# Kernel tuning notes

Hardware: AMD Instinct MI355X
Metric: run time of the kernel (lower is better)

Reference implementation:

```python
import jax, jax.numpy as jnp
import numpy as np

ALPHA = 1.0
EPS = 1e-6


def setup_inputs() -> dict:
    key = jax.random.key(0)
    ks = jax.random.split(key, 6)
    B, d_lat, hidden, n_genes = 256, 32, 512, 4000
    z = jax.random.normal(ks[0], (B, d_lat), dtype=jnp.float32)
    W1 = jax.random.normal(ks[1], (d_lat, hidden), dtype=jnp.float32) / np.sqrt(d_lat)
    b1 = jnp.zeros((hidden,), dtype=jnp.float32)
    W2 = jax.random.normal(ks[2], (hidden, n_genes), dtype=jnp.float32) / np.sqrt(hidden)
    b2 = jnp.zeros((n_genes,), dtype=jnp.float32)
    log_theta = 0.5 * jax.random.normal(ks[3], (n_genes,), dtype=jnp.float32)
    return {"z": z, "W1": W1, "b1": b1, "W2": W2, "b2": b2, "log_theta": log_theta}


def _decode_mu(z_vec, W1, b1, W2, b2):
    # NB decoder mean for a single latent vector; lib_dummy == 1 so no scaling.
    h = jax.nn.relu(z_vec @ W1 + b1)            # [hidden]
    return jax.nn.softplus(h @ W2 + b2)          # [n_genes]


def reference(z, W1, b1, W2, b2, log_theta):
    d_lat = z.shape[1]
    theta = jnp.exp(log_theta)                   # [G], per-gene dispersion

    f = lambda zv: _decode_mu(zv, W1, b1, W2, b2)

    mu = jax.vmap(f)(z)                          # [B, G]
    J = jax.vmap(jax.jacfwd(f))(z)               # [B, G, d_lat]

    # weights computed under no_grad in the original
    mu_ng = jax.lax.stop_gradient(mu)
    weights = theta / (mu_ng * (mu_ng + theta) + EPS)   # [B, G]

    # Gram[b, i, j] = sum_g J[b,g,i] * w[b,g] * J[b,g,j]  (== U @ U.T with U = sqrt(w)*J^T)
    Gram = jnp.einsum('bgi,bg,bgj->bij', J, weights, J)  # [B, d_lat, d_lat]

    eye = jnp.eye(d_lat, dtype=z.dtype)
    losses = jnp.sum((Gram - ALPHA * eye) ** 2, axis=(1, 2))  # [B]
    return jnp.mean(losses)
```

## Files before the change

### kernel.cpp

```cpp
#include <hip/hip_runtime.h>

typedef __bf16 bf16x8 __attribute__((ext_vector_type(8)));
typedef float f32x4 __attribute__((ext_vector_type(4)));
typedef unsigned short u16x8 __attribute__((ext_vector_type(8)));

typedef const void __attribute__((address_space(1)))* gas_ptr;
typedef void __attribute__((address_space(3)))* las_ptr;

#define GLOAD16(gp, lp) __builtin_amdgcn_global_load_lds((gas_ptr)(gp), (las_ptr)(lp), 16, 0, 0)

__device__ __forceinline__ unsigned short f2bf(float f) {
  unsigned int u = __float_as_uint(f);
  u += 0x7FFF + ((u >> 16) & 1);
  return (unsigned short)(u >> 16);
}
__device__ __forceinline__ float bf2f(unsigned short u) {
  return __uint_as_float(((unsigned int)u) << 16);
}

__global__ __launch_bounds__(256) void k_w2t(const float* __restrict__ W2,
                                             unsigned short* __restrict__ W2T) {
  __shared__ float tile[64][65];
  const int gt = blockIdx.x;
  const int jt = blockIdx.y;
  const int t = threadIdx.x;
  const int c = t & 63, r4 = t >> 6;
#pragma unroll
  for (int r = 0; r < 16; ++r) {
    int jj = r * 4 + r4;
    int g = gt * 64 + c;
    tile[jj][c] = (g < 4000) ? W2[(size_t)(jt * 64 + jj) * 4000 + g] : 0.f;
  }
  __syncthreads();
#pragma unroll
  for (int r = 0; r < 16; ++r) {
    int gg = r * 4 + r4;
    W2T[(size_t)(gt * 64 + gg) * 512 + jt * 64 + c] = f2bf(tile[c][gg]);
  }
}

__global__ __launch_bounds__(256) void k_mask(const float* __restrict__ z,
                                              const float* __restrict__ W1,
                                              const float* __restrict__ b1,
                                              unsigned char* __restrict__ maskb,
                                              unsigned short* __restrict__ Hb) {
  __shared__ float zs[32];
  const int b = blockIdx.x, t = threadIdx.x;
  if (t < 32) zs[t] = z[b * 32 + t];
  __syncthreads();
#pragma unroll
  for (int jj = 0; jj < 2; ++jj) {
    int j = t + jj * 256;
    float a = b1[j];
#pragma unroll
    for (int i = 0; i < 32; ++i) a = fmaf(zs[i], W1[i * 512 + j], a);
    bool m = a > 0.f;
    maskb[b * 512 + j] = m ? 1 : 0;
    Hb[b * 512 + j] = m ? f2bf(a) : (unsigned short)0;
  }
}

__global__ __launch_bounds__(256) void k_abig(const float* __restrict__ W1,
                                              const unsigned char* __restrict__ maskb,
                                              unsigned short* __restrict__ Astack) {
  const int b = blockIdx.x, t = threadIdx.x;
#pragma unroll
  for (int k = 0; k < 8; ++k) {
    int c8 = t + k * 256;
    int row = c8 >> 6;
    int k8 = (c8 & 63) * 8;
    unsigned long long m8 = *(const unsigned long long*)(maskb + b * 512 + k8);
    const float* w = W1 + row * 512 + k8;
    u16x8 out;
#pragma unroll
    for (int e = 0; e < 8; ++e)
      out[e] = ((m8 >> (e * 8)) & 0xffULL) ? f2bf(w[e]) : (unsigned short)0;
    *(u16x8*)(Astack + ((size_t)(b * 32 + row)) * 512 + k8) = out;
  }
}

__global__ __launch_bounds__(256) void k_s(const unsigned short* __restrict__ Hb,
                                           const unsigned short* __restrict__ W2T,
                                           const float* __restrict__ b2,
                                           const float* __restrict__ log_theta,
                                           float* __restrict__ Cw) {
  __shared__ __align__(16) char smem[49152];
  char* Abuf = smem;
  char* Bbuf = smem + 16384;

  const int bm = blockIdx.x;
  const int g0 = blockIdx.y * 128;
  const int t = threadIdx.x;
  const int lane = t & 63;
  const int wave = t >> 6;
  const int l8 = lane >> 3;
  const int kxor = (((lane & 7) ^ l8) << 3);
  const int c16 = lane & 15;
  const int lg = lane >> 4;

  f32x4 acc[4][2];
#pragma unroll
  for (int mt = 0; mt < 4; ++mt)
#pragma unroll
    for (int nt = 0; nt < 2; ++nt) acc[mt][nt] = (f32x4){0.f, 0.f, 0.f, 0.f};

#define STAGE_S(buf, kt)                                                              \
  do {                                                                                \
    _Pragma("unroll") for (int qq = 0; qq < 2; ++qq) {                                \
      int q = wave * 2 + qq;                                                          \
      GLOAD16(Hb + (size_t)(bm * 64 + q * 8 + l8) * 512 + (kt) * 64 + kxor,           \
              Abuf + (buf) * 8192 + q * 1024);                                        \
    }                                                                                 \
    _Pragma("unroll") for (int qq = 0; qq < 4; ++qq) {                                \
      int q = wave * 4 + qq;                                                          \
      GLOAD16(W2T + (size_t)(g0 + q * 8 + l8) * 512 + (kt) * 64 + kxor,               \
              Bbuf + (buf) * 16384 + q * 1024);                                       \
    }                                                                                 \
  } while (0)

  STAGE_S(0, 0);
  __syncthreads();

  for (int kt = 0; kt < 8; ++kt) {
    int cur = kt & 1;
    if (kt < 7) STAGE_S(cur ^ 1, kt + 1);
    const char* Ab = Abuf + cur * 8192;
    const char* Bb = Bbuf + cur * 16384;
#pragma unroll
    for (int ks = 0; ks < 2; ++ks) {
      int kb = ks * 64 + lg * 16;
      bf16x8 av[4], bv[2];
#pragma unroll
      for (int mt = 0; mt < 4; ++mt) {
        int row = mt * 16 + c16;
        av[mt] = *(const bf16x8*)(Ab + (row >> 3) * 1024 + (row & 7) * 128 + (kb ^ ((row & 7) << 4)));
      }
#pragma unroll
      for (int nt = 0; nt < 2; ++nt) {
        int row = wave * 32 + nt * 16 + c16;
        bv[nt] = *(const bf16x8*)(Bb + (row >> 3) * 1024 + (row & 7) * 128 + (kb ^ ((row & 7) << 4)));
      }
#pragma unroll
      for (int mt = 0; mt < 4; ++mt)
#pragma unroll
        for (int nt = 0; nt < 2; ++nt)
          acc[mt][nt] = __builtin_amdgcn_mfma_f32_16x16x32_bf16(av[mt], bv[nt], acc[mt][nt], 0, 0, 0);
    }
    __syncthreads();
  }

#pragma unroll
  for (int nt = 0; nt < 2; ++nt) {
    int g = g0 + wave * 32 + nt * 16 + c16;
    if (g < 4000) {
      float bb = b2[g];
      float theta = expf(log_theta[g]);
#pragma unroll
      for (int mt = 0; mt < 4; ++mt)
#pragma unroll
        for (int r = 0; r < 4; ++r) {
          int sample = bm * 64 + mt * 16 + lg * 4 + r;
          float s = acc[mt][nt][r] + bb;
          float sig = 1.f / (1.f + expf(-s));
          float mu = (s > 20.f) ? s : log1pf(expf(s));
          float w = theta / (mu * (mu + theta) + 1e-6f);
          Cw[(size_t)sample * 4096 + g] = w * sig * sig;
        }
    } else {
#pragma unroll
      for (int mt = 0; mt < 4; ++mt)
#pragma unroll
        for (int r = 0; r < 4; ++r) {
          int sample = bm * 64 + mt * 16 + lg * 4 + r;
          Cw[(size_t)sample * 4096 + g] = 0.f;
        }
    }
  }
}

__global__ __launch_bounds__(256, 2) void k_gemm(const unsigned short* __restrict__ Astack,
                                                 const unsigned short* __restrict__ W2T,
                                                 const float* __restrict__ Cw,
                                                 float* __restrict__ Gram) {
  __shared__ __align__(16) char smem[65536];
  char* AbufB = smem;
  char* BbufB = smem + 32768;

  const int bm = blockIdx.x;
  const int g0 = blockIdx.y * 128;
  const int t = threadIdx.x;
  const int lane = t & 63;
  const int wave = t >> 6;
  const int wr = wave >> 1, wc = wave & 1;
  const int l8 = lane >> 3;
  const int kxor = (((lane & 7) ^ l8) << 3);
  const int c16 = lane & 15;
  const int lg = lane >> 4;

  f32x4 acc[4][4];
#pragma unroll
  for (int mt = 0; mt < 4; ++mt)
#pragma unroll
    for (int nt = 0; nt < 4; ++nt) acc[mt][nt] = (f32x4){0.f, 0.f, 0.f, 0.f};

  const size_t Abase = (size_t)bm * 128 * 512;

#define STAGE_G(buf, kt)                                                              \
  do {                                                                                \
    _Pragma("unroll") for (int qq = 0; qq < 4; ++qq) {                                \
      int q = wave * 4 + qq;                                                          \
      GLOAD16(Astack + Abase + (size_t)(q * 8 + l8) * 512 + (kt) * 64 + kxor,         \
              AbufB + (buf) * 16384 + q * 1024);                                      \
    }                                                                                 \
    _Pragma("unroll") for (int qq = 0; qq < 4; ++qq) {                                \
      int q = wave * 4 + qq;                                                          \
      GLOAD16(W2T + (size_t)(g0 + q * 8 + l8) * 512 + (kt) * 64 + kxor,               \
              BbufB + (buf) * 16384 + q * 1024);                                      \
    }                                                                                 \
  } while (0)

  STAGE_G(0, 0);
  __syncthreads();

  for (int kt = 0; kt < 8; ++kt) {
    int cur = kt & 1;
    if (kt < 7) STAGE_G(cur ^ 1, kt + 1);
    const char* Ab = AbufB + cur * 16384;
    const char* Bb = BbufB + cur * 16384;
#pragma unroll
    for (int ks = 0; ks < 2; ++ks) {
      int kb = ks * 64 + lg * 16;
      bf16x8 av[4], bv[4];
#pragma unroll
      for (int mt = 0; mt < 4; ++mt) {
        int row = wr * 64 + mt * 16 + c16;
        av[mt] = *(const bf16x8*)(Ab + (row >> 3) * 1024 + (row & 7) * 128 + (kb ^ ((row & 7) << 4)));
      }
#pragma unroll
      for (int nt = 0; nt < 4; ++nt) {
        int row = wc * 64 + nt * 16 + c16;
        bv[nt] = *(const bf16x8*)(Bb + (row >> 3) * 1024 + (row & 7) * 128 + (kb ^ ((row & 7) << 4)));
      }
#pragma unroll
      for (int mt = 0; mt < 4; ++mt)
#pragma unroll
        for (int nt = 0; nt < 4; ++nt)
          acc[mt][nt] = __builtin_amdgcn_mfma_f32_16x16x32_bf16(av[mt], bv[nt], acc[mt][nt], 0, 0, 0);
    }
    __syncthreads();
  }

  unsigned short* T = (unsigned short*)smem;
  float* c_lds = (float*)(smem + 34816);

#pragma unroll
  for (int mt = 0; mt < 4; ++mt)
#pragma unroll
    for (int nt = 0; nt < 4; ++nt)
#pragma unroll
      for (int r = 0; r < 4; ++r) {
        int row = wr * 64 + mt * 16 + lg * 4 + r;
        int col = wc * 64 + nt * 16 + c16;
        T[row * 136 + col] = f2bf(acc[mt][nt][r]);
      }
#pragma unroll
  for (int k = 0; k < 2; ++k) {
    int e = t + k * 256;
    c_lds[e] = Cw[(size_t)(bm * 4 + (e >> 7)) * 4096 + g0 + (e & 127)];
  }
  __syncthreads();

  {
    const int s = wave;
    f32x4 gacc[2][2];
#pragma unroll
    for (int m2 = 0; m2 < 2; ++m2)
#pragma unroll
      for (int n2 = 0; n2 < 2; ++n2) gacc[m2][n2] = (f32x4){0.f, 0.f, 0.f, 0.f};

#pragma unroll
    for (int ch = 0; ch < 4; ++ch) {
      u16x8 raw[2];
      bf16x8 ap[2], bp[2];
      f32x4 cv0 = *(const f32x4*)(c_lds + s * 128 + ch * 32 + lg * 8);
      f32x4 cv1 = *(const f32x4*)(c_lds + s * 128 + ch * 32 + lg * 8 + 4);
#pragma unroll
      for (int m2 = 0; m2 < 2; ++m2) {
        int row = s * 32 + m2 * 16 + c16;
        raw[m2] = *(const u16x8*)((const char*)T + row * 272 + ch * 64 + lg * 16);
        u16x8 sc;
#pragma unroll
        for (int e = 0; e < 4; ++e) sc[e] = f2bf(bf2f(raw[m2][e]) * cv0[e]);
#pragma unroll
        for (int e = 0; e < 4; ++e) sc[4 + e] = f2bf(bf2f(raw[m2][4 + e]) * cv1[e]);
        ap[m2] = __builtin_bit_cast(bf16x8, sc);
        bp[m2] = __builtin_bit_cast(bf16x8, raw[m2]);
      }
#pragma unroll
      for (int m2 = 0; m2 < 2; ++m2)
#pragma unroll
        for (int n2 = 0; n2 < 2; ++n2)
          gacc[m2][n2] = __builtin_amdgcn_mfma_f32_16x16x32_bf16(ap[m2], bp[n2], gacc[m2][n2], 0, 0, 0);
    }

#pragma unroll
    for (int m2 = 0; m2 < 2; ++m2)
#pragma unroll
      for (int n2 = 0; n2 < 2; ++n2)
#pragma unroll
        for (int r = 0; r < 4; ++r) {
          int i = m2 * 16 + lg * 4 + r;
          int j = n2 * 16 + c16;
          atomicAdd(Gram + (size_t)(bm * 4 + s) * 1024 + i * 32 + j, gacc[m2][n2][r]);
        }
  }
}

__global__ __launch_bounds__(256) void k_loss(const float* __restrict__ Gram,
                                              float* __restrict__ out) {
  __shared__ float red[4];
  const int b = blockIdx.x, t = threadIdx.x;
  float local = 0.f;
#pragma unroll
  for (int k = 0; k < 4; ++k) {
    int e = t + k * 256;
    float d = Gram[(size_t)b * 1024 + e] - (((e >> 5) == (e & 31)) ? 1.f : 0.f);
    local += d * d;
  }
#pragma unroll
  for (int off = 32; off > 0; off >>= 1) local += __shfl_down(local, off);
  if ((t & 63) == 0) red[t >> 6] = local;
  __syncthreads();
  if (t == 0) {
    float s = red[0] + red[1] + red[2] + red[3];
    atomicAdd(out, s * (1.f / 256.f));
  }
}

extern "C" void kernel_launch(void* const* d_in, const int* in_sizes, int n_in,
                              void* d_out, int out_size, void* d_ws, size_t ws_size,
                              hipStream_t stream) {
  const float* z = (const float*)d_in[0];
  const float* W1 = (const float*)d_in[1];
  const float* b1 = (const float*)d_in[2];
  const float* W2 = (const float*)d_in[3];
  const float* b2 = (const float*)d_in[4];
  const float* lt = (const float*)d_in[5];

  char* ws = (char*)d_ws;
  unsigned short* W2T = (unsigned short*)ws;
  unsigned short* Astack = (unsigned short*)(ws + 4194304);
  unsigned short* Hb = (unsigned short*)(ws + 12582912);
  unsigned char* maskb = (unsigned char*)(ws + 12845056);
  float* Cw = (float*)(ws + 12976128);
  float* Gram = (float*)(ws + 17170432);

  hipMemsetAsync(Gram, 0, 256 * 1024 * 4, stream);
  hipMemsetAsync(d_out, 0, 4, stream);

  k_w2t<<<dim3(64, 8), 256, 0, stream>>>(W2, W2T);
  k_mask<<<256, 256, 0, stream>>>(z, W1, b1, maskb, Hb);
  k_abig<<<256, 256, 0, stream>>>(W1, maskb, Astack);
  k_s<<<dim3(4, 32), 256, 0, stream>>>(Hb, W2T, b2, lt, Cw);
  k_gemm<<<dim3(64, 32), 256, 0, stream>>>(Astack, W2T, Cw, Gram);
  k_loss<<<256, 256, 0, stream>>>(Gram, (float*)d_out);
}
```

Baseline: 166.0 us.

## Rewrite pre-activation GEMM as per-wave register tiles without LDS staging

Replaces the LDS-staged, double-buffered 64x128 block GEMM in the weight-computation kernel with a per-wave 16x32 tile. Each wave keeps its full K slice of A in registers and streams B directly from global memory. The grid grows from 128 blocks to 512 blocks, so more CUs have work and the LDS and barrier overhead goes away. The cost is less data reuse across waves, more global and L2 traffic for W2T, and higher register pressure from holding 16 A vectors.

Result: faster. 159.9 us (-3.7%).

```diff
diff --git a/kernel.cpp b/kernel.cpp
--- a/kernel.cpp
+++ b/kernel.cpp
@@ -79,101 +79,62 @@
   }
 }
 
-__global__ __launch_bounds__(256) void k_s(const unsigned short* __restrict__ Hb,
-                                           const unsigned short* __restrict__ W2T,
-                                           const float* __restrict__ b2,
-                                           const float* __restrict__ log_theta,
-                                           float* __restrict__ Cw) {
-  __shared__ __align__(16) char smem[49152];
-  char* Abuf = smem;
-  char* Bbuf = smem + 16384;
-
-  const int bm = blockIdx.x;
-  const int g0 = blockIdx.y * 128;
+__global__ __launch_bounds__(256) void k_s2(const unsigned short* __restrict__ Hb,
+                                            const unsigned short* __restrict__ W2T,
+                                            const float* __restrict__ b2,
+                                            const float* __restrict__ log_theta,
+                                            float* __restrict__ Cw) {
   const int t = threadIdx.x;
   const int lane = t & 63;
   const int wave = t >> 6;
-  const int l8 = lane >> 3;
-  const int kxor = (((lane & 7) ^ l8) << 3);
-  const int c16 = lane & 15;
-  const int lg = lane >> 4;
-
-  f32x4 acc[4][2];
-#pragma unroll
-  for (int mt = 0; mt < 4; ++mt)
-#pragma unroll
-    for (int nt = 0; nt < 2; ++nt) acc[mt][nt] = (f32x4){0.f, 0.f, 0.f, 0.f};
-
-#define STAGE_S(buf, kt)                                                              \
-  do {                                                                                \
-    _Pragma("unroll") for (int qq = 0; qq < 2; ++qq) {                                \
-      int q = wave * 2 + qq;                                                          \
-      GLOAD16(Hb + (size_t)(bm * 64 + q * 8 + l8) * 512 + (kt) * 64 + kxor,           \
-              Abuf + (buf) * 8192 + q * 1024);                                        \
-    }                                                                                 \
-    _Pragma("unroll") for (int qq = 0; qq < 4; ++qq) {                                \
-      int q = wave * 4 + qq;                                                          \
-      GLOAD16(W2T + (size_t)(g0 + q * 8 + l8) * 512 + (kt) * 64 + kxor,               \
-              Bbuf + (buf) * 16384 + q * 1024);                                       \
-    }                                                                                 \
-  } while (0)
-
-  STAGE_S(0, 0);
-  __syncthreads();
-
-  for (int kt = 0; kt < 8; ++kt) {
-    int cur = kt & 1;
-    if (kt < 7) STAGE_S(cur ^ 1, kt + 1);
-    const char* Ab = Abuf + cur * 8192;
-    const char* Bb = Bbuf + cur * 16384;
-#pragma unroll
-    for (int ks = 0; ks < 2; ++ks) {
-      int kb = ks * 64 + lg * 16;
-      bf16x8 av[4], bv[2];
-#pragma unroll
-      for (int mt = 0; mt < 4; ++mt) {
-        int row = mt * 16 + c16;
-        av[mt] = *(const bf16x8*)(Ab + (row >> 3) * 1024 + (row & 7) * 128 + (kb ^ ((row & 7) << 4)));
-      }
-#pragma unroll
-      for (int nt = 0; nt < 2; ++nt) {
-        int row = wave * 32 + nt * 16 + c16;
-        bv[nt] = *(const bf16x8*)(Bb + (row >> 3) * 1024 + (row & 7) * 128 + (kb ^ ((row & 7) << 4)));
-      }
-#pragma unroll
-      for (int mt = 0; mt < 4; ++mt)
-#pragma unroll
-        for (int nt = 0; nt < 2; ++nt)
-          acc[mt][nt] = __builtin_amdgcn_mfma_f32_16x16x32_bf16(av[mt], bv[nt], acc[mt][nt], 0, 0, 0);
-    }
-    __syncthreads();
-  }
-
-#pragma unroll
-  for (int nt = 0; nt < 2; ++nt) {
-    int g = g0 + wave * 32 + nt * 16 + c16;
+  const int wid = blockIdx.x * 4 + wave;
+  const int st = wid >> 7;
+  const int gt = wid & 127;
+  const int c16 = lane & 15, lg = lane >> 4;
+  const int s0 = st * 16, g0 = gt * 32;
+
+  bf16x8 av[16];
+  {
+    const unsigned short* Arow = Hb + (size_t)(s0 + c16) * 512 + lg * 8;
+#pragma unroll
+    for (int ks = 0; ks < 16; ++ks) av[ks] = *(const bf16x8*)(Arow + ks * 32);
+  }
+
+  f32x4 acc[2];
+  acc[0] = (f32x4){0.f, 0.f, 0.f, 0.f};
+  acc[1] = (f32x4){0.f, 0.f, 0.f, 0.f};
+
+  const unsigned short* B0 = W2T + (size_t)(g0 + c16) * 512 + lg * 8;
+  const unsigned short* B1 = B0 + 16 * 512;
+#pragma unroll
+  for (int ks = 0; ks < 16; ++ks) {
+    bf16x8 b0 = *(const bf16x8*)(B0 + ks * 32);
+    bf16x8 b1 = *(const bf16x8*)(B1 + ks * 32);
+    acc[0] = __builtin_amdgcn_mfma_f32_16x16x32_bf16(av[ks], b0, acc[0], 0, 0, 0);
+    acc[1] = __builtin_amdgcn_mfma_f32_16x16x32_bf16(av[ks], b1, acc[1], 0, 0, 0);
+  }
+
+#pragma unroll
+  for (int n = 0; n < 2; ++n) {
+    int g = g0 + n * 16 + c16;
     if (g < 4000) {
       float bb = b2[g];
       float theta = expf(log_theta[g]);
 #pragma unroll
-      for (int mt = 0; mt < 4; ++mt)
-#pragma unroll
-        for (int r = 0; r < 4; ++r) {
-          int sample = bm * 64 + mt * 16 + lg * 4 + r;
-          float s = acc[mt][nt][r] + bb;
-          float sig = 1.f / (1.f + expf(-s));
-          float mu = (s > 20.f) ? s : log1pf(expf(s));
-          float w = theta / (mu * (mu + theta) + 1e-6f);
-          Cw[(size_t)sample * 4096 + g] = w * sig * sig;
-        }
+      for (int r = 0; r < 4; ++r) {
+        int sample = s0 + lg * 4 + r;
+        float s = acc[n][r] + bb;
+        float sig = 1.f / (1.f + expf(-s));
+        float mu = (s > 20.f) ? s : log1pf(expf(s));
+        float w = theta / (mu * (mu + theta) + 1e-6f);
+        Cw[(size_t)sample * 4096 + g] = w * sig * sig;
+      }
     } else {
 #pragma unroll
-      for (int mt = 0; mt < 4; ++mt)
-#pragma unroll
-        for (int r = 0; r < 4; ++r) {
-          int sample = bm * 64 + mt * 16 + lg * 4 + r;
-          Cw[(size_t)sample * 4096 + g] = 0.f;
-        }
+      for (int r = 0; r < 4; ++r) {
+        int sample = s0 + lg * 4 + r;
+        Cw[(size_t)sample * 4096 + g] = 0.f;
+      }
     }
   }
 }
@@ -361,7 +322,7 @@
   k_w2t<<<dim3(64, 8), 256, 0, stream>>>(W2, W2T);
   k_mask<<<256, 256, 0, stream>>>(z, W1, b1, maskb, Hb);
   k_abig<<<256, 256, 0, stream>>>(W1, maskb, Astack);
-  k_s<<<dim3(4, 32), 256, 0, stream>>>(Hb, W2T, b2, lt, Cw);
+  k_s2<<<512, 256, 0, stream>>>(Hb, W2T, b2, lt, Cw);
   k_gemm<<<dim3(64, 32), 256, 0, stream>>>(Astack, W2T, Cw, Gram);
   k_loss<<<256, 256, 0, stream>>>(Gram, (float*)d_out);
 }
```
